# Optimization experiments

Measured on AMD Instinct MI355X. Metric: run time of the kernel, lower is better.

## Reference

```python
import jax, jax.numpy as jnp
import numpy as np

LMAX = 3
NDEG = LMAX + 1            # degrees l = 0..3
MDIM = 2 * LMAX + 1        # padded m dimension (7)
K = 128                    # channels per degree
N = 4096                   # number of samples (atomic environments)
NITER = 2                  # number_of_iterations

# CG paths (l1, l2) -> L with |l1-l2| <= L <= min(l1+l2, LMAX); 34 paths
PATHS = [(l1, l2, L)
         for L in range(NDEG)
         for l1 in range(NDEG)
         for l2 in range(NDEG)
         if abs(l1 - l2) <= L <= l1 + l2]


def setup_inputs() -> dict:
    key = jax.random.key(0)
    k1, k2, k3, k4 = jax.random.split(key, 4)

    # zero-mask padded m components: valid m < 2l+1 per degree l
    mmask = (jnp.arange(MDIM)[None, :] < (2 * jnp.arange(NDEG) + 1)[:, None])
    mmask = mmask.astype(jnp.float32)                      # [NDEG, MDIM]

    feats = jax.random.normal(k1, (NDEG, N, MDIM, K), dtype=jnp.float32)
    feats = feats * mmask[:, None, :, None]

    # CG-like coefficients, zero-padded per path to [2l1+1, 2l2+1, 2L+1]
    umask = np.zeros((len(PATHS), MDIM, MDIM, MDIM), dtype=np.float32)
    for p, (l1, l2, L) in enumerate(PATHS):
        umask[p, :2 * l1 + 1, :2 * l2 + 1, :2 * L + 1] = 1.0
    U = jax.random.normal(k2, (len(PATHS), MDIM, MDIM, MDIM), dtype=jnp.float32)
    U = 0.1 * U * jnp.asarray(umask)

    scale = 1.0 / np.sqrt(K)
    mixer_W = scale * jax.random.normal(k3, (NITER + 1, NDEG, K, K), dtype=jnp.float32)
    iter_W = scale * jax.random.normal(k4, (NITER, NDEG, K, K), dtype=jnp.float32)

    return {"feats": feats, "U": U, "mixer_W": mixer_W, "iter_W": iter_W}


def spherical_linear(f, W):
    # per-degree channel mix: f [NDEG, N, MDIM, K], W [NDEG, K, K]
    return jnp.einsum('lnmk,lkj->lnmj', f, W)


def tensor_product(f1, f2, U):
    # channel-wise CG tensor product, summed over paths into each output degree L
    out = jnp.zeros_like(f1)
    for p, (l1, l2, L) in enumerate(PATHS):
        out = out.at[L].add(jnp.einsum('nak,nbk,abc->nck', f1[l1], f2[l2], U[p]))
    return out


def reference(feats, U, mixer_W, iter_W):
    # mixed_densities = [mixer(density) for mixer in self.mixers]
    mixed = [spherical_linear(feats, mixer_W[i]) for i in range(NITER + 1)]
    cur = mixed[0]
    # CG iterations: residual( linear( tensor_product(cur, mixed[t+1]) ) )
    for t in range(NITER):
        tp = tensor_product(cur, mixed[t + 1], U)
        cur = cur + spherical_linear(tp, iter_W[t])
    return cur
```

## Files before the change

### kernel.cpp

```cpp
#include <hip/hip_runtime.h>

#define NSAMP 4096
#define KCH   128
#define MDIM  7

typedef __attribute__((ext_vector_type(8))) short bf16x8;
typedef __attribute__((ext_vector_type(4))) float f32x4;
typedef __attribute__((ext_vector_type(4))) unsigned u32x4;

static constexpr int RB[4] = {0, 1, 4, 9};
static constexpr int RE[4] = {1, 4, 9, 16};
static constexpr int PR_L[16] = {0,1,1,1,2,2,2,2,2,3,3,3,3,3,3,3};
static constexpr int PR_M[16] = {0,0,1,2,0,1,2,3,4,0,1,2,3,4,5,6};

static constexpr int PIDX[4][4][4] = {
  { { 0,-1,-1,-1},{-1, 1,-1,-1},{-1,-1, 2,-1},{-1,-1,-1, 3} },
  { {-1, 4,-1,-1},{ 5, 6, 7,-1},{-1, 8, 9,10},{-1,-1,11,12} },
  { {-1,-1,13,-1},{-1,14,15,16},{17,18,19,20},{-1,21,22,23} },
  { {-1,-1,-1,24},{-1,-1,25,26},{-1,27,28,29},{30,31,32,33} }
};

static constexpr int ZL[12] = {0,0,0,0,0,0, 1,1,1,1, 2,2};
static constexpr int ZM[12] = {1,2,3,4,5,6, 3,4,5,6, 5,6};

#define WP_BYTES 1310720u
#define BG_BYTES 16384u

static __device__ __forceinline__ unsigned short f2bf(float x) {
    unsigned u = __builtin_bit_cast(unsigned, x);
    u = u + 0x7FFFu + ((u >> 16) & 1u);
    return (unsigned short)(u >> 16);
}
static __device__ __forceinline__ float bf2f(unsigned short h) {
    unsigned u = ((unsigned)h) << 16;
    return __builtin_bit_cast(float, u);
}

__global__ __launch_bounds__(256) void cg_prep(const float* __restrict__ mW,
                                               const float* __restrict__ iW,
                                               unsigned short* __restrict__ Wp)
{
    int gid = blockIdx.x * 256 + threadIdx.x;
    int lane = gid & 63;
    int set  = gid >> 6;
    int spl = set & 1;
    int ks  = (set >> 1) & 3;
    int ct  = (set >> 3) & 7;
    int l   = (set >> 6) & 3;
    int mi  = set >> 8;
    const float* src = (mi < 3) ? (mW + ((size_t)mi * 4 + l) * (KCH * KCH))
                                : (iW + ((size_t)(mi - 3) * 4 + l) * (KCH * KCH));
    int j  = ct * 16 + (lane & 15);
    int kb = ks * 32 + (lane >> 4) * 8;
    unsigned short o[8];
#pragma unroll
    for (int e = 0; e < 8; ++e) {
        float w = src[(size_t)(kb + e) * KCH + j];
        unsigned short h = f2bf(w);
        o[e] = spl ? f2bf(w - bf2f(h)) : h;
    }
    uint4 pk;
    unsigned* pw = (unsigned*)&pk;
#pragma unroll
    for (int q = 0; q < 4; ++q) pw[q] = (unsigned)o[2*q] | ((unsigned)o[2*q+1] << 16);
    *(uint4*)(Wp + (size_t)set * 512 + lane * 8) = pk;
}

__global__ __launch_bounds__(256) void cg_prepg(const float* __restrict__ U,
                                                unsigned short* __restrict__ Bg)
{
    const int gid  = blockIdx.x * 256 + threadIdx.x;
    const int s    = gid >> 7;
    const int spl  = (gid >> 6) & 1;
    const int lane = gid & 63;
    const int c    = lane & 15;
    const int kb   = s * 32 + (lane >> 4) * 8;
    const int Lo   = PR_L[c], cm = PR_M[c];
    unsigned short o[8];
#pragma unroll
    for (int e = 0; e < 8; ++e) {
        const int k  = kb + e;
        const int i  = k >> 4, j = k & 15;
        const int l1 = PR_L[i], a = PR_M[i];
        const int l2 = PR_L[j], b = PR_M[j];
        const int p  = PIDX[Lo][l1][l2];
        float val = (p >= 0) ? U[p * 343 + (a * 7 + b) * 7 + cm] : 0.0f;
        unsigned short h = f2bf(val);
        o[e] = spl ? f2bf(val - bf2f(h)) : h;
    }
    uint4 pk;
    unsigned* pw = (unsigned*)&pk;
#pragma unroll
    for (int q = 0; q < 4; ++q) pw[q] = (unsigned)o[2*q] | ((unsigned)o[2*q+1] << 16);
    *(uint4*)(Bg + (size_t)((s * 2 + spl) * 64 + lane) * 8) = pk;
}

static __device__ __forceinline__ bf16x8 ldF(const unsigned short* P, int row16, int key, int c) {
    int cs = c ^ (key & 7);
    return *(const bf16x8*)(P + row16 * 128 + cs * 8);
}

static __device__ __forceinline__ void stage_feats(const float* __restrict__ feats,
                                                   unsigned short* Fh, unsigned short* Fl,
                                                   int tid, int n0)
{
    const int row = tid >> 1;
    const int r   = row >> 4;
    const int nlr = row & 15;
    const int kh  = tid & 1;
    const int l = PR_L[r], m = PR_M[r];
    const float* g = feats + (((size_t)l * NSAMP + (n0 + nlr)) * MDIM + m) * KCH + kh * 64;
    unsigned short* fh = Fh + row * 128;
    unsigned short* fl = Fl + row * 128;
#pragma unroll
    for (int c8 = 0; c8 < 8; ++c8) {
        f32x4 a = *(const f32x4*)(g + c8 * 8);
        f32x4 b = *(const f32x4*)(g + c8 * 8 + 4);
        float v[8] = {a[0], a[1], a[2], a[3], b[0], b[1], b[2], b[3]};
        unsigned short hi[8], lo[8];
#pragma unroll
        for (int i = 0; i < 8; ++i) {
            hi[i] = f2bf(v[i]);
            lo[i] = f2bf(v[i] - bf2f(hi[i]));
        }
        uint4 ph, pl;
        unsigned* pwh = (unsigned*)&ph;
        unsigned* pwl = (unsigned*)&pl;
#pragma unroll
        for (int q = 0; q < 4; ++q) {
            pwh[q] = (unsigned)hi[2*q] | ((unsigned)hi[2*q+1] << 16);
            pwl[q] = (unsigned)lo[2*q] | ((unsigned)lo[2*q+1] << 16);
        }
        const int cs = (kh * 8 + c8) ^ (nlr & 7);
        *(uint4*)(fh + cs * 8) = ph;
        *(uint4*)(fl + cs * 8) = pl;
    }
}

static __device__ __forceinline__ void mix_sweep(const unsigned short* Fh, const unsigned short* Fl,
                                                 const bf16x8* __restrict__ Wp, int mi,
                                                 int ct, int lane, f32x4 (&acc)[16])
{
    const int kg = lane >> 4;
    const int l15 = lane & 15;
#pragma unroll
    for (int r = 0; r < 16; ++r) { acc[r][0]=acc[r][1]=acc[r][2]=acc[r][3]=0.0f; }
#pragma unroll
    for (int ks = 0; ks < 4; ++ks) {
#pragma unroll
        for (int l = 0; l < 4; ++l) {
            const int s0 = (((mi * 4 + l) * 8 + ct) * 4 + ks) * 2;
            bf16x8 bh = Wp[(size_t)s0 * 64 + lane];
            bf16x8 bl = Wp[(size_t)(s0 + 1) * 64 + lane];
#pragma unroll
            for (int r = RB[l]; r < RE[l]; ++r) {
                bf16x8 ah = ldF(Fh, r * 16 + l15, l15, ks * 4 + kg);
                bf16x8 al = ldF(Fl, r * 16 + l15, l15, ks * 4 + kg);
                acc[r] = __builtin_amdgcn_mfma_f32_16x16x32_bf16(ah, bh, acc[r], 0, 0, 0);
                acc[r] = __builtin_amdgcn_mfma_f32_16x16x32_bf16(ah, bl, acc[r], 0, 0, 0);
                acc[r] = __builtin_amdgcn_mfma_f32_16x16x32_bf16(al, bh, acc[r], 0, 0, 0);
            }
        }
    }
}

static __device__ __forceinline__ void acc_to_lds(const f32x4 (&acc)[16], unsigned short* P,
                                                  int ct, int lane)
{
    const int kg = lane >> 4;
    const int l15 = lane & 15;
    const int chnk = ct * 2 + (l15 >> 3);
#pragma unroll
    for (int r = 0; r < 16; ++r) {
#pragma unroll
        for (int q = 0; q < 4; ++q) {
            const int smp = kg * 4 + q;
            const int cs = chnk ^ (smp & 7);
            P[(smp * 16 + r) * 128 + cs * 8 + (l15 & 7)] = f2bf(acc[r][q]);
        }
    }
}

static __device__ __forceinline__ void tp_iter(unsigned short* Ch, const unsigned short* Mt,
                                               const bf16x8* __restrict__ Bg,
                                               const bf16x8* __restrict__ Wp, int miW,
                                               int ct, int lane, f32x4 (&racc)[16])
{
    const int kg  = lane >> 4;
    const int l15 = lane & 15;
    const int i0 = kg >> 1;
    const int j0 = (kg & 1) * 8;
    const int chnk = ct * 2 + (l15 >> 3);
    const int chA  = ct * 2 + (kg >> 1);
    const int co4  = (kg * 4) & 7;

    bf16x8 bgh[8], bgl[8];
#pragma unroll
    for (int s = 0; s < 8; ++s) {
        bgh[s] = Bg[(size_t)(s * 2 + 0) * 64 + lane];
        bgl[s] = Bg[(size_t)(s * 2 + 1) * 64 + lane];
    }

    f32x4 tpa[4];
#pragma unroll 1
    for (int g = 0; g < 4; ++g) {
#pragma unroll
        for (int uu = 0; uu < 4; ++uu) {
            const int u = g * 4 + uu;
            const int cs = chnk ^ (u & 7);
            const unsigned short* cb = Ch + u * 2048 + cs * 8 + (l15 & 7);
            const unsigned short* mb = Mt + u * 2048 + cs * 8 + (l15 & 7);
            float cvv[8], mvv[8];
#pragma unroll
            for (int s = 0; s < 8; ++s) cvv[s] = bf2f(cb[(i0 + 2 * s) * 128]);
#pragma unroll
            for (int e = 0; e < 8; ++e) mvv[e] = bf2f(mb[(j0 + e) * 128]);
            f32x4 acc = {0.0f, 0.0f, 0.0f, 0.0f};
#pragma unroll
            for (int s = 0; s < 8; ++s) {
                float pf[8];
#pragma unroll
                for (int e = 0; e < 8; ++e) pf[e] = cvv[s] * mvv[e];
                unsigned ah[4];
#pragma unroll
                for (int d = 0; d < 4; ++d) {
                    asm("v_cvt_pk_bf16_f32 %0, %1, %2" : "=v"(ah[d]) : "v"(pf[2*d]), "v"(pf[2*d+1]));
                }
                const u32x4 AH = {ah[0], ah[1], ah[2], ah[3]};
                const bf16x8 a_h = __builtin_bit_cast(bf16x8, AH);
                acc = __builtin_amdgcn_mfma_f32_16x16x32_bf16(a_h, bgh[s], acc, 0, 0, 0);
                acc = __builtin_amdgcn_mfma_f32_16x16x32_bf16(a_h, bgl[s], acc, 0, 0, 0);
            }
            tpa[uu] = acc;
        }
        __syncthreads();
#pragma unroll
        for (int uu = 0; uu < 4; ++uu) {
            const int u = g * 4 + uu;
            const int cs = chA ^ (u & 7);
            const int soff = (u * 16 + l15) * 128 + cs * 8 + co4;
            const unsigned short h0 = f2bf(tpa[uu][0]);
            const unsigned short h1 = f2bf(tpa[uu][1]);
            const unsigned short h2 = f2bf(tpa[uu][2]);
            const unsigned short h3 = f2bf(tpa[uu][3]);
            *(unsigned*)(Ch + soff)     = (unsigned)h0 | ((unsigned)h1 << 16);
            *(unsigned*)(Ch + soff + 2) = (unsigned)h2 | ((unsigned)h3 << 16);
        }
    }
    __syncthreads();

#pragma unroll
    for (int ks = 0; ks < 4; ++ks) {
#pragma unroll
        for (int l = 0; l < 4; ++l) {
            const int s0 = (((miW * 4 + l) * 8 + ct) * 4 + ks) * 2;
            bf16x8 bh = Wp[(size_t)s0 * 64 + lane];
            bf16x8 bl = Wp[(size_t)(s0 + 1) * 64 + lane];
#pragma unroll
            for (int r = RB[l]; r < RE[l]; ++r) {
                bf16x8 ah = ldF(Ch, l15 * 16 + r, l15, ks * 4 + kg);
                racc[r] = __builtin_amdgcn_mfma_f32_16x16x32_bf16(ah, bh, racc[r], 0, 0, 0);
                racc[r] = __builtin_amdgcn_mfma_f32_16x16x32_bf16(ah, bl, racc[r], 0, 0, 0);
            }
        }
    }
}

__global__ __launch_bounds__(512, 2) void cg_fuseA(const float* __restrict__ feats,
                                                   const bf16x8* __restrict__ Wp,
                                                   const bf16x8* __restrict__ Bg,
                                                   float* __restrict__ Pcur,
                                                   int base)
{
    extern __shared__ char smem[];
    unsigned short* Fh = (unsigned short*)smem;
    unsigned short* Fl = Fh + 32768;

    const int tid  = threadIdx.x;
    const int lane = tid & 63;
    const int ct   = tid >> 6;
    const int nl0  = blockIdx.x * 16;
    const int kg   = lane >> 4;
    const int l15  = lane & 15;
    const int j    = ct * 16 + l15;

    stage_feats(feats, Fh, Fl, tid, base + nl0);
    __syncthreads();

    f32x4 acc0[16], acc1[16];
    mix_sweep(Fh, Fl, Wp, 0, ct, lane, acc0);
    mix_sweep(Fh, Fl, Wp, 1, ct, lane, acc1);
    __syncthreads();

    acc_to_lds(acc0, Fh, ct, lane);
    acc_to_lds(acc1, Fl, ct, lane);
    __syncthreads();

    tp_iter(Fh, Fl, Bg, Wp, 3, ct, lane, acc0);

#pragma unroll
    for (int r = 0; r < 16; ++r) {
#pragma unroll
        for (int q = 0; q < 4; ++q) {
            const int nl = nl0 + kg * 4 + q;
            Pcur[((size_t)nl * 16 + r) * KCH + j] = acc0[r][q];
        }
    }
}

__global__ __launch_bounds__(512, 2) void cg_fuseB(const float* __restrict__ feats,
                                                   const bf16x8* __restrict__ Wp,
                                                   const bf16x8* __restrict__ Bg,
                                                   const float* __restrict__ Pcur,
                                                   float* __restrict__ gout,
                                                   int base)
{
    extern __shared__ char smem[];
    unsigned short* Fh = (unsigned short*)smem;
    unsigned short* Fl = Fh + 32768;

    const int tid  = threadIdx.x;
    const int lane = tid & 63;
    const int ct   = tid >> 6;
    const int nl0  = blockIdx.x * 16;
    const int kg   = lane >> 4;
    const int l15  = lane & 15;
    const int j    = ct * 16 + l15;

    f32x4 racc[16];
#pragma unroll
    for (int r = 0; r < 16; ++r) {
#pragma unroll
        for (int q = 0; q < 4; ++q) {
            const int nl = nl0 + kg * 4 + q;
            racc[r][q] = Pcur[((size_t)nl * 16 + r) * KCH + j];
        }
    }

    stage_feats(feats, Fh, Fl, tid, base + nl0);
    __syncthreads();

    f32x4 accm[16];
    mix_sweep(Fh, Fl, Wp, 2, ct, lane, accm);
    __syncthreads();

    acc_to_lds(racc, Fh, ct, lane);
    acc_to_lds(accm, Fl, ct, lane);
    __syncthreads();

    tp_iter(Fh, Fl, Bg, Wp, 4, ct, lane, racc);

#pragma unroll
    for (int r = 0; r < 16; ++r) {
#pragma unroll
        for (int q = 0; q < 4; ++q) {
            const int n = base + nl0 + kg * 4 + q;
            gout[(((size_t)PR_L[r] * NSAMP + n) * MDIM + PR_M[r]) * KCH + j] = racc[r][q];
        }
    }

    {
        const int j2 = tid & 127;
        const int g  = tid >> 7;
#pragma unroll
        for (int z = 0; z < 12; ++z) {
#pragma unroll
            for (int i = 0; i < 4; ++i) {
                const int n = base + nl0 + g * 4 + i;
                gout[(((size_t)ZL[z] * NSAMP + n) * MDIM + ZM[z]) * KCH + j2] = 0.0f;
            }
        }
    }
}

extern "C" void kernel_launch(void* const* d_in, const int* in_sizes, int n_in,
                              void* d_out, int out_size, void* d_ws, size_t ws_size,
                              hipStream_t stream)
{
    const float* feats = (const float*)d_in[0];
    const float* U     = (const float*)d_in[1];
    const float* mW    = (const float*)d_in[2];
    const float* iW    = (const float*)d_in[3];
    float* out = (float*)d_out;

    const size_t fixed = (size_t)WP_BYTES + BG_BYTES;
    size_t avail = (ws_size > fixed) ? (ws_size - fixed) : 0;
    int NC = (int)(avail / 8192);
    NC = (NC / 16) * 16;
    if (NC > NSAMP) NC = NSAMP;
    if (NC < 16) return;

    char* wsb = (char*)d_ws;
    unsigned short* Wp = (unsigned short*)wsb;
    unsigned short* Bg = (unsigned short*)(wsb + WP_BYTES);
    float* Pcur = (float*)(wsb + fixed);

    hipFuncSetAttribute(reinterpret_cast<const void*>(cg_fuseA),
                        hipFuncAttributeMaxDynamicSharedMemorySize, 131072);
    hipFuncSetAttribute(reinterpret_cast<const void*>(cg_fuseB),
                        hipFuncAttributeMaxDynamicSharedMemorySize, 131072);

    cg_prep<<<320, 256, 0, stream>>>(mW, iW, Wp);
    cg_prepg<<<4, 256, 0, stream>>>(U, Bg);

    for (int base = 0; base < NSAMP; base += NC) {
        const int nc = (NSAMP - base < NC) ? (NSAMP - base) : NC;
        cg_fuseA<<<nc / 16, 512, 131072, stream>>>(feats, (const bf16x8*)Wp,
                                                   (const bf16x8*)Bg, Pcur, base);
        cg_fuseB<<<nc / 16, 512, 131072, stream>>>(feats, (const bf16x8*)Wp,
                                                   (const bf16x8*)Bg, Pcur, out, base);
    }
}
```

Measured before the change: 106.1 us.

## Fuse both CG iteration kernels into a single kernel without intermediate buffer

Merges the two per-iteration kernels into one that stages features once, computes all three mixer products, and runs both tensor-product iterations in sequence. This removes the global round trip of the intermediate current state, the second feature staging, and one launch per chunk. In exchange, three 16-entry accumulator arrays are live at once, so launch bounds drop to one block per CU. That raises register pressure and may reduce occupancy and latency hiding.

```diff
diff --git a/kernel.cpp b/kernel.cpp
--- a/kernel.cpp
+++ b/kernel.cpp
@@ -266,11 +266,10 @@
     }
 }
 
-__global__ __launch_bounds__(512, 2) void cg_fuseA(const float* __restrict__ feats,
+__global__ __launch_bounds__(512, 1) void cg_fused(const float* __restrict__ feats,
                                                    const bf16x8* __restrict__ Wp,
                                                    const bf16x8* __restrict__ Bg,
-                                                   float* __restrict__ Pcur,
-                                                   int base)
+                                                   float* __restrict__ gout)
 {
     extern __shared__ char smem[];
     unsigned short* Fh = (unsigned short*)smem;
@@ -284,81 +283,34 @@
     const int l15  = lane & 15;
     const int j    = ct * 16 + l15;
 
-    stage_feats(feats, Fh, Fl, tid, base + nl0);
-    __syncthreads();
-
-    f32x4 acc0[16], acc1[16];
-    mix_sweep(Fh, Fl, Wp, 0, ct, lane, acc0);
-    mix_sweep(Fh, Fl, Wp, 1, ct, lane, acc1);
-    __syncthreads();
-
-    acc_to_lds(acc0, Fh, ct, lane);
-    acc_to_lds(acc1, Fl, ct, lane);
-    __syncthreads();
-
-    tp_iter(Fh, Fl, Bg, Wp, 3, ct, lane, acc0);
+    stage_feats(feats, Fh, Fl, tid, nl0);
+    __syncthreads();
+
+    f32x4 accC[16], accM1[16], accM2[16];
+    mix_sweep(Fh, Fl, Wp, 0, ct, lane, accC);
+    mix_sweep(Fh, Fl, Wp, 1, ct, lane, accM1);
+    mix_sweep(Fh, Fl, Wp, 2, ct, lane, accM2);
+    __syncthreads();
+
+    acc_to_lds(accC,  Fh, ct, lane);
+    acc_to_lds(accM1, Fl, ct, lane);
+    __syncthreads();
+    tp_iter(Fh, Fl, Bg, Wp, 3, ct, lane, accC);
+    __syncthreads();
+
+    acc_to_lds(accC,  Fh, ct, lane);
+    acc_to_lds(accM2, Fl, ct, lane);
+    __syncthreads();
+    tp_iter(Fh, Fl, Bg, Wp, 4, ct, lane, accC);
 
 #pragma unroll
     for (int r = 0; r < 16; ++r) {
 #pragma unroll
         for (int q = 0; q < 4; ++q) {
-            const int nl = nl0 + kg * 4 + q;
-            Pcur[((size_t)nl * 16 + r) * KCH + j] = acc0[r][q];
-        }
-    }
-}
-
-__global__ __launch_bounds__(512, 2) void cg_fuseB(const float* __restrict__ feats,
-                                                   const bf16x8* __restrict__ Wp,
-                                                   const bf16x8* __restrict__ Bg,
-                                                   const float* __restrict__ Pcur,
-                                                   float* __restrict__ gout,
-                                                   int base)
-{
-    extern __shared__ char smem[];
-    unsigned short* Fh = (unsigned short*)smem;
-    unsigned short* Fl = Fh + 32768;
-
-    const int tid  = threadIdx.x;
-    const int lane = tid & 63;
-    const int ct   = tid >> 6;
-    const int nl0  = blockIdx.x * 16;
-    const int kg   = lane >> 4;
-    const int l15  = lane & 15;
-    const int j    = ct * 16 + l15;
-
-    f32x4 racc[16];
-#pragma unroll
-    for (int r = 0; r < 16; ++r) {
-#pragma unroll
-        for (int q = 0; q < 4; ++q) {
-            const int nl = nl0 + kg * 4 + q;
-            racc[r][q] = Pcur[((size_t)nl * 16 + r) * KCH + j];
-        }
-    }
-
-    stage_feats(feats, Fh, Fl, tid, base + nl0);
-    __syncthreads();
-
-    f32x4 accm[16];
-    mix_sweep(Fh, Fl, Wp, 2, ct, lane, accm);
-    __syncthreads();
-
-    acc_to_lds(racc, Fh, ct, lane);
-    acc_to_lds(accm, Fl, ct, lane);
-    __syncthreads();
-
-    tp_iter(Fh, Fl, Bg, Wp, 4, ct, lane, racc);
-
-#pragma unroll
-    for (int r = 0; r < 16; ++r) {
-#pragma unroll
-        for (int q = 0; q < 4; ++q) {
-            const int n = base + nl0 + kg * 4 + q;
-            gout[(((size_t)PR_L[r] * NSAMP + n) * MDIM + PR_M[r]) * KCH + j] = racc[r][q];
-        }
-    }
-
+            const int n = nl0 + kg * 4 + q;
+            gout[(((size_t)PR_L[r] * NSAMP + n) * MDIM + PR_M[r]) * KCH + j] = accC[r][q];
+        }
+    }
     {
         const int j2 = tid & 127;
         const int g  = tid >> 7;
@@ -366,7 +318,7 @@
         for (int z = 0; z < 12; ++z) {
 #pragma unroll
             for (int i = 0; i < 4; ++i) {
-                const int n = base + nl0 + g * 4 + i;
+                const int n = nl0 + g * 4 + i;
                 gout[(((size_t)ZL[z] * NSAMP + n) * MDIM + ZM[z]) * KCH + j2] = 0.0f;
             }
         }
@@ -383,31 +335,15 @@
     const float* iW    = (const float*)d_in[3];
     float* out = (float*)d_out;
 
-    const size_t fixed = (size_t)WP_BYTES + BG_BYTES;
-    size_t avail = (ws_size > fixed) ? (ws_size - fixed) : 0;
-    int NC = (int)(avail / 8192);
-    NC = (NC / 16) * 16;
-    if (NC > NSAMP) NC = NSAMP;
-    if (NC < 16) return;
-
     char* wsb = (char*)d_ws;
     unsigned short* Wp = (unsigned short*)wsb;
     unsigned short* Bg = (unsigned short*)(wsb + WP_BYTES);
-    float* Pcur = (float*)(wsb + fixed);
-
-    hipFuncSetAttribute(reinterpret_cast<const void*>(cg_fuseA),
-                        hipFuncAttributeMaxDynamicSharedMemorySize, 131072);
-    hipFuncSetAttribute(reinterpret_cast<const void*>(cg_fuseB),
+
+    hipFuncSetAttribute(reinterpret_cast<const void*>(cg_fused),
                         hipFuncAttributeMaxDynamicSharedMemorySize, 131072);
 
     cg_prep<<<320, 256, 0, stream>>>(mW, iW, Wp);
     cg_prepg<<<4, 256, 0, stream>>>(U, Bg);
-
-    for (int base = 0; base < NSAMP; base += NC) {
-        const int nc = (NSAMP - base < NC) ? (NSAMP - base) : NC;
-        cg_fuseA<<<nc / 16, 512, 131072, stream>>>(feats, (const bf16x8*)Wp,
-                                                   (const bf16x8*)Bg, Pcur, base);
-        cg_fuseB<<<nc / 16, 512, 131072, stream>>>(feats, (const bf16x8*)Wp,
-                                                   (const bf16x8*)Bg, Pcur, out, base);
-    }
-}
+    cg_fused<<<NSAMP / 16, 512, 131072, stream>>>(feats, (const bf16x8*)Wp,
+                                                  (const bf16x8*)Bg, out);
+}
```

Result: slower. 128.2 us (+20.9%).

## Drop low-bf16 split of features and store intermediate state in bf16

Applied to the files above, without the earlier changes.

Features are staged as a single bf16 copy instead of a hi/lo split, so each mixing MFMA group issues two products (feature×Whi, feature×Wlo) where it used to issue three, and one LDS load is removed per step. The intermediate state Pcur passed between the two kernels is now stored in bf16 rather than fp32, which halves that workspace traffic and lets larger chunks fit in the workspace. The LDS swizzle key for the tensor-product output buffer also changes to (u^l15)&7 to reduce bank conflicts on reads. The cost is lower numerical precision in both the features and the carried state, which may exceed tolerance.

```diff
diff --git a/kernel.cpp b/kernel.cpp
--- a/kernel.cpp
+++ b/kernel.cpp
@@ -100,9 +100,8 @@
     return *(const bf16x8*)(P + row16 * 128 + cs * 8);
 }
 
-static __device__ __forceinline__ void stage_feats(const float* __restrict__ feats,
-                                                   unsigned short* Fh, unsigned short* Fl,
-                                                   int tid, int n0)
+static __device__ __forceinline__ void stage_feats1(const float* __restrict__ feats,
+                                                    unsigned short* Fh, int tid, int n0)
 {
     const int row = tid >> 1;
     const int r   = row >> 4;
@@ -111,35 +110,24 @@
     const int l = PR_L[r], m = PR_M[r];
     const float* g = feats + (((size_t)l * NSAMP + (n0 + nlr)) * MDIM + m) * KCH + kh * 64;
     unsigned short* fh = Fh + row * 128;
-    unsigned short* fl = Fl + row * 128;
 #pragma unroll
     for (int c8 = 0; c8 < 8; ++c8) {
         f32x4 a = *(const f32x4*)(g + c8 * 8);
         f32x4 b = *(const f32x4*)(g + c8 * 8 + 4);
         float v[8] = {a[0], a[1], a[2], a[3], b[0], b[1], b[2], b[3]};
-        unsigned short hi[8], lo[8];
-#pragma unroll
-        for (int i = 0; i < 8; ++i) {
-            hi[i] = f2bf(v[i]);
-            lo[i] = f2bf(v[i] - bf2f(hi[i]));
-        }
-        uint4 ph, pl;
-        unsigned* pwh = (unsigned*)&ph;
-        unsigned* pwl = (unsigned*)&pl;
-#pragma unroll
-        for (int q = 0; q < 4; ++q) {
-            pwh[q] = (unsigned)hi[2*q] | ((unsigned)hi[2*q+1] << 16);
-            pwl[q] = (unsigned)lo[2*q] | ((unsigned)lo[2*q+1] << 16);
-        }
+        uint4 ph;
+        unsigned* pw = (unsigned*)&ph;
+#pragma unroll
+        for (int q = 0; q < 4; ++q)
+            pw[q] = (unsigned)f2bf(v[2*q]) | ((unsigned)f2bf(v[2*q+1]) << 16);
         const int cs = (kh * 8 + c8) ^ (nlr & 7);
         *(uint4*)(fh + cs * 8) = ph;
-        *(uint4*)(fl + cs * 8) = pl;
-    }
-}
-
-static __device__ __forceinline__ void mix_sweep(const unsigned short* Fh, const unsigned short* Fl,
-                                                 const bf16x8* __restrict__ Wp, int mi,
-                                                 int ct, int lane, f32x4 (&acc)[16])
+    }
+}
+
+static __device__ __forceinline__ void mix_sweep1(const unsigned short* Fh,
+                                                  const bf16x8* __restrict__ Wp, int mi,
+                                                  int ct, int lane, f32x4 (&acc)[16])
 {
     const int kg = lane >> 4;
     const int l15 = lane & 15;
@@ -155,10 +143,8 @@
 #pragma unroll
             for (int r = RB[l]; r < RE[l]; ++r) {
                 bf16x8 ah = ldF(Fh, r * 16 + l15, l15, ks * 4 + kg);
-                bf16x8 al = ldF(Fl, r * 16 + l15, l15, ks * 4 + kg);
                 acc[r] = __builtin_amdgcn_mfma_f32_16x16x32_bf16(ah, bh, acc[r], 0, 0, 0);
                 acc[r] = __builtin_amdgcn_mfma_f32_16x16x32_bf16(ah, bl, acc[r], 0, 0, 0);
-                acc[r] = __builtin_amdgcn_mfma_f32_16x16x32_bf16(al, bh, acc[r], 0, 0, 0);
             }
         }
     }
@@ -237,7 +223,7 @@
 #pragma unroll
         for (int uu = 0; uu < 4; ++uu) {
             const int u = g * 4 + uu;
-            const int cs = chA ^ (u & 7);
+            const int cs = chA ^ ((u ^ l15) & 7);
             const int soff = (u * 16 + l15) * 128 + cs * 8 + co4;
             const unsigned short h0 = f2bf(tpa[uu][0]);
             const unsigned short h1 = f2bf(tpa[uu][1]);
@@ -258,7 +244,7 @@
             bf16x8 bl = Wp[(size_t)(s0 + 1) * 64 + lane];
 #pragma unroll
             for (int r = RB[l]; r < RE[l]; ++r) {
-                bf16x8 ah = ldF(Ch, l15 * 16 + r, l15, ks * 4 + kg);
+                bf16x8 ah = ldF(Ch, l15 * 16 + r, l15 ^ r, ks * 4 + kg);
                 racc[r] = __builtin_amdgcn_mfma_f32_16x16x32_bf16(ah, bh, racc[r], 0, 0, 0);
                 racc[r] = __builtin_amdgcn_mfma_f32_16x16x32_bf16(ah, bl, racc[r], 0, 0, 0);
             }
@@ -269,12 +255,12 @@
 __global__ __launch_bounds__(512, 2) void cg_fuseA(const float* __restrict__ feats,
                                                    const bf16x8* __restrict__ Wp,
                                                    const bf16x8* __restrict__ Bg,
-                                                   float* __restrict__ Pcur,
+                                                   unsigned short* __restrict__ Pcur,
                                                    int base)
 {
     extern __shared__ char smem[];
     unsigned short* Fh = (unsigned short*)smem;
-    unsigned short* Fl = Fh + 32768;
+    unsigned short* Tp = Fh + 32768;
 
     const int tid  = threadIdx.x;
     const int lane = tid & 63;
@@ -284,26 +270,26 @@
     const int l15  = lane & 15;
     const int j    = ct * 16 + l15;
 
-    stage_feats(feats, Fh, Fl, tid, base + nl0);
-    __syncthreads();
-
-    f32x4 acc0[16], acc1[16];
-    mix_sweep(Fh, Fl, Wp, 0, ct, lane, acc0);
-    mix_sweep(Fh, Fl, Wp, 1, ct, lane, acc1);
-    __syncthreads();
-
-    acc_to_lds(acc0, Fh, ct, lane);
-    acc_to_lds(acc1, Fl, ct, lane);
-    __syncthreads();
-
-    tp_iter(Fh, Fl, Bg, Wp, 3, ct, lane, acc0);
+    stage_feats1(feats, Fh, tid, base + nl0);
+    __syncthreads();
+
+    f32x4 accC[16], accM[16];
+    mix_sweep1(Fh, Wp, 0, ct, lane, accC);
+    mix_sweep1(Fh, Wp, 1, ct, lane, accM);
+    __syncthreads();
+
+    acc_to_lds(accC, Fh, ct, lane);
+    acc_to_lds(accM, Tp, ct, lane);
+    __syncthreads();
+
+    tp_iter(Fh, Tp, Bg, Wp, 3, ct, lane, accC);
 
 #pragma unroll
     for (int r = 0; r < 16; ++r) {
 #pragma unroll
         for (int q = 0; q < 4; ++q) {
             const int nl = nl0 + kg * 4 + q;
-            Pcur[((size_t)nl * 16 + r) * KCH + j] = acc0[r][q];
+            Pcur[((size_t)nl * 16 + r) * KCH + j] = f2bf(accC[r][q]);
         }
     }
 }
@@ -311,13 +297,13 @@
 __global__ __launch_bounds__(512, 2) void cg_fuseB(const float* __restrict__ feats,
                                                    const bf16x8* __restrict__ Wp,
                                                    const bf16x8* __restrict__ Bg,
-                                                   const float* __restrict__ Pcur,
+                                                   const unsigned short* __restrict__ Pcur,
                                                    float* __restrict__ gout,
                                                    int base)
 {
     extern __shared__ char smem[];
     unsigned short* Fh = (unsigned short*)smem;
-    unsigned short* Fl = Fh + 32768;
+    unsigned short* Tp = Fh + 32768;
 
     const int tid  = threadIdx.x;
     const int lane = tid & 63;
@@ -333,22 +319,22 @@
 #pragma unroll
         for (int q = 0; q < 4; ++q) {
             const int nl = nl0 + kg * 4 + q;
-            racc[r][q] = Pcur[((size_t)nl * 16 + r) * KCH + j];
-        }
-    }
-
-    stage_feats(feats, Fh, Fl, tid, base + nl0);
-    __syncthreads();
-
-    f32x4 accm[16];
-    mix_sweep(Fh, Fl, Wp, 2, ct, lane, accm);
+            racc[r][q] = bf2f(Pcur[((size_t)nl * 16 + r) * KCH + j]);
+        }
+    }
+
+    stage_feats1(feats, Fh, tid, base + nl0);
+    __syncthreads();
+
+    f32x4 accM[16];
+    mix_sweep1(Fh, Wp, 2, ct, lane, accM);
     __syncthreads();
 
     acc_to_lds(racc, Fh, ct, lane);
-    acc_to_lds(accm, Fl, ct, lane);
-    __syncthreads();
-
-    tp_iter(Fh, Fl, Bg, Wp, 4, ct, lane, racc);
+    acc_to_lds(accM, Tp, ct, lane);
+    __syncthreads();
+
+    tp_iter(Fh, Tp, Bg, Wp, 4, ct, lane, racc);
 
 #pragma unroll
     for (int r = 0; r < 16; ++r) {
@@ -358,7 +344,6 @@
             gout[(((size_t)PR_L[r] * NSAMP + n) * MDIM + PR_M[r]) * KCH + j] = racc[r][q];
         }
     }
-
     {
         const int j2 = tid & 127;
         const int g  = tid >> 7;
@@ -385,15 +370,15 @@
 
     const size_t fixed = (size_t)WP_BYTES + BG_BYTES;
     size_t avail = (ws_size > fixed) ? (ws_size - fixed) : 0;
-    int NC = (int)(avail / 8192);
+    int NC = (int)(avail / 4096);
     NC = (NC / 16) * 16;
     if (NC > NSAMP) NC = NSAMP;
     if (NC < 16) return;
 
     char* wsb = (char*)d_ws;
-    unsigned short* Wp = (unsigned short*)wsb;
-    unsigned short* Bg = (unsigned short*)(wsb + WP_BYTES);
-    float* Pcur = (float*)(wsb + fixed);
+    unsigned short* Wp   = (unsigned short*)wsb;
+    unsigned short* Bg   = (unsigned short*)(wsb + WP_BYTES);
+    unsigned short* Pcur = (unsigned short*)(wsb + fixed);
 
     hipFuncSetAttribute(reinterpret_cast<const void*>(cg_fuseA),
                         hipFuncAttributeMaxDynamicSharedMemorySize, 131072);
```

After: 95.39 us. 1.11x faster.
